# Kernel tuning notes

Measured on AMD Instinct MI355X. Metric: run time of the kernel, lower is better.

## Reference

```python
import jax, jax.numpy as jnp
import numpy as np

SIMS = 16
AMP = 1.0  # cfg['attention_amplifier']


def setup_inputs() -> dict:
    key = jax.random.key(0)
    k1, k2, k3 = jax.random.split(key, 3)
    B, F = 32, 2048
    data = jax.random.normal(k1, (B * SIMS, F), dtype=jnp.float32)
    attention = jax.random.normal(k2, (B * SIMS, F), dtype=jnp.float32)
    W = jax.random.normal(k3, (SIMS, 2 * SIMS), dtype=jnp.float32) * (1.0 / np.sqrt(2 * SIMS))
    b = jnp.zeros((SIMS,), dtype=jnp.float32)
    return {"data": data, "attention": attention, "W": W, "b": b}


def reference(data, attention, W, b):
    s = SIMS
    B = data.shape[0] // s
    inputs = data.reshape(B, s, -1)            # [B, s, F]
    attn_in = attention.reshape(B, s, -1)      # [B, s, G]
    # bmm(inputs^T, attention) -> [B, F, G]
    a = jnp.einsum('bsf,bsg->bfg', inputs, attn_in)
    a = jax.nn.log_softmax(a, axis=1)          # log_softmax over F dim (dim=1)
    # bmm(a, attention^T) -> [B, F, s]
    a = jnp.einsum('bfg,bsg->bfs', a, attn_in)
    concat = jnp.concatenate([jnp.swapaxes(a, 1, 2), inputs], axis=1)  # [B, 2s, F]
    concat = jnp.swapaxes(concat, 1, 2).reshape(-1, 2 * s)             # [B*F, 2s]
    gate = jax.nn.sigmoid(concat @ W.T + b)    # [B*F, s]
    # output.t().contiguous().view(data.shape): [s, B*F] row-major -> [B*s, F]
    gate = gate.T.reshape(data.shape)
    return gate * data * AMP
```

## Files before the change

kernel.cpp:

```cpp
#include <hip/hip_runtime.h>
#include <math.h>

#define LOG2E 1.44269504088896340736f
#define LN2   0.69314718055994530942f

typedef _Float16 half8 __attribute__((ext_vector_type(8)));
typedef float f32x4v __attribute__((ext_vector_type(4)));

#define AROW 24

template <bool ATOMIC>
__global__ __launch_bounds__(256, 4) void kA(const float* __restrict__ data,
                                             const float* __restrict__ attn,
                                             float* __restrict__ Lout) {
    __shared__ _Float16 AhB[128 * AROW];
    __shared__ _Float16 AlB[128 * AROW];
    const int tid = threadIdx.x;
    const int lin = blockIdx.x;
    const int b = lin & 31, fb = (lin >> 5) & 3, gb = lin >> 7;
    const int wave = tid >> 6, lane = tid & 63;
    const int n = lane & 15, q = lane >> 4;
    const int s0 = (q & 1) * 8;

    const float* Tb = attn + (size_t)b * 16 * 2048;
    half8 B1[2], B2[2];
#pragma unroll
    for (int ct = 0; ct < 2; ++ct) {
        const int g = gb * 128 + wave * 32 + ct * 16 + n;
        half8 bh, bl;
#pragma unroll
        for (int j = 0; j < 8; ++j) {
            float x = Tb[(size_t)(s0 + j) * 2048 + g] * LOG2E;
            _Float16 h = (_Float16)x;
            _Float16 l = (_Float16)(x - (float)h);
            bh[j] = h;
            bl[j] = (q < 2) ? l : (_Float16)0.0f;
        }
        B1[ct] = bh;
        B2[ct] = bl;
    }

    f32x4v cs0 = {0.f, 0.f, 0.f, 0.f}, cs1 = {0.f, 0.f, 0.f, 0.f};

    const float* Ab = data + (size_t)b * 16 * 2048 + fb * 512;
    const int fst = tid & 127;
    const int sh  = (tid >> 7) * 8;
    const _Float16* aptr = ((q < 2) ? AhB : AlB) + n * AROW + s0;

    float x[8];
#pragma unroll
    for (int j = 0; j < 8; ++j) x[j] = Ab[(size_t)(sh + j) * 2048 + fst];

    for (int chunk = 0; chunk < 4; ++chunk) {
        half8 hv, lv;
#pragma unroll
        for (int j = 0; j < 8; ++j) {
            float v = x[j];
            _Float16 h = (_Float16)v;
            hv[j] = h;
            lv[j] = (_Float16)(v - (float)h);
        }
        __syncthreads();
        *(half8*)(AhB + fst * AROW + sh) = hv;
        *(half8*)(AlB + fst * AROW + sh) = lv;
        __syncthreads();

        if (chunk < 3) {
            const float* Ac = Ab + (chunk + 1) * 128;
#pragma unroll
            for (int j = 0; j < 8; ++j) x[j] = Ac[(size_t)(sh + j) * 2048 + fst];
        }

#pragma unroll
        for (int rt = 0; rt < 8; ++rt) {
            half8 af = *(const half8*)(aptr + rt * 16 * AROW);
            f32x4v C = {0.f, 0.f, 0.f, 0.f};
            C = __builtin_amdgcn_mfma_f32_16x16x32_f16(af, B1[0], C, 0, 0, 0);
            C = __builtin_amdgcn_mfma_f32_16x16x32_f16(af, B2[0], C, 0, 0, 0);
            cs0[0] += __builtin_amdgcn_exp2f(C[0]);
            cs0[1] += __builtin_amdgcn_exp2f(C[1]);
            cs0[2] += __builtin_amdgcn_exp2f(C[2]);
            cs0[3] += __builtin_amdgcn_exp2f(C[3]);
            f32x4v D = {0.f, 0.f, 0.f, 0.f};
            D = __builtin_amdgcn_mfma_f32_16x16x32_f16(af, B1[1], D, 0, 0, 0);
            D = __builtin_amdgcn_mfma_f32_16x16x32_f16(af, B2[1], D, 0, 0, 0);
            cs1[0] += __builtin_amdgcn_exp2f(D[0]);
            cs1[1] += __builtin_amdgcn_exp2f(D[1]);
            cs1[2] += __builtin_amdgcn_exp2f(D[2]);
            cs1[3] += __builtin_amdgcn_exp2f(D[3]);
        }
    }

    float v0 = cs0[0] + cs0[1] + cs0[2] + cs0[3];
    float v1 = cs1[0] + cs1[1] + cs1[2] + cs1[3];
    v0 += __shfl_xor(v0, 16);
    v0 += __shfl_xor(v0, 32);
    v1 += __shfl_xor(v1, 16);
    v1 += __shfl_xor(v1, 32);
    if (q == 0) {
        const int g = gb * 128 + wave * 32 + n;
        if (ATOMIC) {
            atomicAdd(&Lout[(size_t)b * 2048 + g], v0);
            atomicAdd(&Lout[(size_t)b * 2048 + g + 16], v1);
        } else {
            Lout[((size_t)fb * 32 + b) * 2048 + g] = v0;
            Lout[((size_t)fb * 32 + b) * 2048 + g + 16] = v1;
        }
    }
}

#define TP2 132
__global__ __launch_bounds__(256) void kTail(const float* __restrict__ attn,
                                             const float* __restrict__ Lpart, int nparts,
                                             float* __restrict__ Mpart,
                                             float* __restrict__ cpart) {
    __shared__ float Tsh[16 * TP2];
    __shared__ float Lsh[128];
    __shared__ float red[16][17];
    const int tid = threadIdx.x;
    const int seg = blockIdx.x, b = blockIdx.y;
    const int g0 = seg * 128;

    {
        const int gcol = tid & 127, sh = (tid >> 7) * 8;
#pragma unroll
        for (int j = 0; j < 8; ++j) {
            const int s = sh + j;
            Tsh[s * TP2 + gcol] = attn[(size_t)(b * 16 + s) * 2048 + g0 + gcol];
        }
    }
    if (tid < 128) {
        float sum = 0.f;
        for (int p = 0; p < nparts; ++p)
            sum += Lpart[((size_t)p * 32 + b) * 2048 + g0 + tid];
        Lsh[tid] = LN2 * __builtin_amdgcn_logf(sum);
    }
    __syncthreads();

    {
        const int t = tid & 15, i = tid >> 4;
        float acc = 0.f;
#pragma unroll
        for (int k = 0; k < 2; ++k) {
            float4 l  = *(const float4*)(Lsh + i * 8 + k * 4);
            float4 tv = *(const float4*)(Tsh + t * TP2 + i * 8 + k * 4);
            acc += l.x * tv.x + l.y * tv.y + l.z * tv.z + l.w * tv.w;
        }
        red[t][i] = acc;
    }
    __syncthreads();
    if (tid < 16) {
        float s = 0.f;
#pragma unroll
        for (int k = 0; k < 16; ++k) s += red[tid][k];
        cpart[((size_t)seg * 32 + b) * 16 + tid] = s;
    }

    {
        const int s = tid >> 4, t = tid & 15;
        float a0 = 0.f, a1 = 0.f;
#pragma unroll 4
        for (int qk = 0; qk < 16; ++qk) {
            float4 x = *(const float4*)(Tsh + s * TP2 + qk * 8);
            float4 y = *(const float4*)(Tsh + t * TP2 + qk * 8);
            a0 += x.x * y.x + x.y * y.y + x.z * y.z + x.w * y.w;
            float4 x2 = *(const float4*)(Tsh + s * TP2 + qk * 8 + 4);
            float4 y2 = *(const float4*)(Tsh + t * TP2 + qk * 8 + 4);
            a1 += x2.x * y2.x + x2.y * y2.y + x2.z * y2.z + x2.w * y2.w;
        }
        Mpart[((size_t)seg * 32 + b) * 256 + tid] = a0 + a1;
    }
}

#define NSEG 16
__global__ __launch_bounds__(256) void kC2(const float* __restrict__ data,
                                           const float* __restrict__ Mpart,
                                           const float* __restrict__ cpart,
                                           const float* __restrict__ W,
                                           const float* __restrict__ bias,
                                           float* __restrict__ out) {
    __shared__ float Msh[256];
    __shared__ float csh[16];
    __shared__ float Vsh[256];
    __shared__ float w0sh[16];
    const int tid = threadIdx.x;
    const int b = blockIdx.y;
    const int f = blockIdx.x * 128 + (tid & 127);
    const int jh = tid >> 7;

    {
        float m = 0.f;
#pragma unroll
        for (int p = 0; p < NSEG; ++p) m += Mpart[((size_t)p * 32 + b) * 256 + tid];
        Msh[tid] = m;
        if (tid < 16) {
            float c = 0.f;
#pragma unroll
            for (int p = 0; p < NSEG; ++p) c += cpart[((size_t)p * 32 + b) * 16 + tid];
            csh[tid] = c;
        }
    }
    __syncthreads();
    {
        const int s = tid >> 4, j = tid & 15;
        float acc = 0.f;
#pragma unroll
        for (int t = 0; t < 16; ++t) acc += Msh[s * 16 + t] * W[j * 32 + t];
        Vsh[s * 16 + j] = acc + W[j * 32 + 16 + s];
        if (s == 0) {
            float w0 = 0.f;
#pragma unroll
            for (int t = 0; t < 16; ++t) w0 += csh[t] * W[j * 32 + t];
            w0sh[j] = bias[j] - w0;
        }
    }
    __syncthreads();

    float As[16];
#pragma unroll
    for (int s = 0; s < 16; ++s)
        As[s] = data[(size_t)(b * 16 + s) * 2048 + f];
#pragma unroll
    for (int jj = 0; jj < 8; ++jj) {
        const int j = jh * 8 + jj;
        float p = w0sh[j];
#pragma unroll
        for (int s = 0; s < 16; ++s) p += As[s] * Vsh[s * 16 + j];
        float e = __builtin_amdgcn_exp2f(-LOG2E * p);
        float gate = __builtin_amdgcn_rcpf(1.0f + e);
        size_t r = (size_t)(j * 32 + b) * 2048 + f;
        out[r] = gate * data[r];
    }
}

extern "C" void kernel_launch(void* const* d_in, const int* in_sizes, int n_in,
                              void* d_out, int out_size, void* d_ws, size_t ws_size,
                              hipStream_t stream) {
    const float* data = (const float*)d_in[0];
    const float* attn = (const float*)d_in[1];
    const float* W    = (const float*)d_in[2];
    const float* bias = (const float*)d_in[3];
    float* out = (float*)d_out;
    float* ws  = (float*)d_ws;

    const size_t LP = 4 * 32 * 2048;
    const size_t MP = NSEG * 32 * 256;
    const size_t CP = NSEG * 32 * 16;
    const size_t need_big = LP + MP + CP;

    if (ws_size >= need_big * sizeof(float)) {
        float* Lpart = ws;
        float* Mpart = ws + LP;
        float* cpart = Mpart + MP;
        kA<false><<<dim3(2048, 1, 1), 256, 0, stream>>>(data, attn, Lpart);
        kTail<<<dim3(16, 32), 256, 0, stream>>>(attn, Lpart, 4, Mpart, cpart);
        kC2<<<dim3(16, 32), 256, 0, stream>>>(data, Mpart, cpart, W, bias, out);
    } else {
        float* Lsum  = ws;
        float* Mpart = ws + 65536;
        float* cpart = Mpart + MP;
        hipMemsetAsync(Lsum, 0, 65536 * sizeof(float), stream);
        kA<true><<<dim3(2048, 1, 1), 256, 0, stream>>>(data, attn, Lsum);
        kTail<<<dim3(16, 32), 256, 0, stream>>>(attn, Lsum, 1, Mpart, cpart);
        kC2<<<dim3(16, 32), 256, 0, stream>>>(data, Mpart, cpart, W, bias, out);
    }
}
```

Before: 94.09 us.

## Precompute fp16 hi/lo MFMA fragments in a prep kernel, drop LDS staging in kA

Adds a prep kernel that splits data and attention into fp16 hi/lo parts once and writes them to workspace, already laid out as MFMA fragments. The main kA kernel then loads fragments straight from global memory, with no LDS staging, no barriers and no per-block conversion. Before, each block redid the split for the data and attention tiles it read, so the same conversions ran many times across blocks. The cost is an extra launch and extra global traffic for the fragment buffers, plus a larger workspace requirement. The old LDS kernel is kept as the fallback when workspace is small.

```diff
diff --git a/kernel.cpp b/kernel.cpp
--- a/kernel.cpp
+++ b/kernel.cpp
@@ -7,12 +7,119 @@
 typedef _Float16 half8 __attribute__((ext_vector_type(8)));
 typedef float f32x4v __attribute__((ext_vector_type(4)));
 
+__global__ __launch_bounds__(256) void kPrep(const float* __restrict__ data,
+                                             const float* __restrict__ attn,
+                                             _Float16* __restrict__ Afrag,
+                                             _Float16* __restrict__ Tfrag) {
+    const int tid = threadIdx.x;
+    const int b = blockIdx.y;
+    const int f = blockIdx.x * 256 + tid;
+
+    _Float16 h16[16], l16[16];
+#pragma unroll
+    for (int s = 0; s < 16; ++s) {
+        float v = data[(size_t)(b * 16 + s) * 2048 + f];
+        _Float16 h = (_Float16)v;
+        h16[s] = h;
+        l16[s] = (_Float16)(v - (float)h);
+    }
+    {
+        const int fb = f >> 9, c = (f >> 7) & 3, rt = (f >> 4) & 7, n = f & 15;
+        _Float16* dst = Afrag + ((size_t)((b * 4 + fb) * 32 + c * 8 + rt)) * 512 + n * 8;
+#pragma unroll
+        for (int qq = 0; qq < 4; ++qq) {
+            const _Float16* src = (qq < 2) ? h16 : l16;
+            const int s0 = (qq & 1) * 8;
+            half8 v;
+#pragma unroll
+            for (int j = 0; j < 8; ++j) v[j] = src[s0 + j];
+            *(half8*)(dst + qq * 128) = v;
+        }
+    }
+
+    _Float16 th[16], tl[16];
+#pragma unroll
+    for (int s = 0; s < 16; ++s) {
+        float v = attn[(size_t)(b * 16 + s) * 2048 + f] * LOG2E;
+        _Float16 h = (_Float16)v;
+        th[s] = h;
+        tl[s] = (_Float16)(v - (float)h);
+    }
+#pragma unroll
+    for (int p = 0; p < 4; ++p) {
+        const _Float16* src = (p < 2) ? th : tl;
+        const int s0 = (p & 1) * 8;
+        half8 v;
+#pragma unroll
+        for (int j = 0; j < 8; ++j) v[j] = src[s0 + j];
+        *(half8*)(Tfrag + ((size_t)(b * 4 + p) * 2048 + f) * 8) = v;
+    }
+}
+
+template <bool ATOMIC>
+__global__ __launch_bounds__(256, 4) void kA(const _Float16* __restrict__ Afrag,
+                                             const _Float16* __restrict__ Tfrag,
+                                             float* __restrict__ Lout) {
+    const int tid = threadIdx.x;
+    const int lin = blockIdx.x;
+    const int gb = lin & 15, b = (lin >> 4) & 31, fb = lin >> 9;
+    const int wave = tid >> 6, lane = tid & 63;
+    const int n = lane & 15, q = lane >> 4;
+
+    half8 B1[2], B2[2];
+    const half8 zero = {};
+#pragma unroll
+    for (int ct = 0; ct < 2; ++ct) {
+        const int g = gb * 128 + wave * 32 + ct * 16 + n;
+        B1[ct] = *(const half8*)(Tfrag + ((size_t)(b * 4 + (q & 1)) * 2048 + g) * 8);
+        half8 b2 = *(const half8*)(Tfrag + ((size_t)(b * 4 + 2 + (q & 1)) * 2048 + g) * 8);
+        B2[ct] = (q < 2) ? b2 : zero;
+    }
+
+    f32x4v cs0 = {0.f, 0.f, 0.f, 0.f}, cs1 = {0.f, 0.f, 0.f, 0.f};
+    const _Float16* Ab = Afrag + ((size_t)((b * 4 + fb) * 32)) * 512 + lane * 8;
+
+#pragma unroll 4
+    for (int rr = 0; rr < 32; ++rr) {
+        half8 af = *(const half8*)(Ab + (size_t)rr * 512);
+        f32x4v C = {0.f, 0.f, 0.f, 0.f};
+        C = __builtin_amdgcn_mfma_f32_16x16x32_f16(af, B1[0], C, 0, 0, 0);
+        C = __builtin_amdgcn_mfma_f32_16x16x32_f16(af, B2[0], C, 0, 0, 0);
+        cs0[0] += __builtin_amdgcn_exp2f(C[0]);
+        cs0[1] += __builtin_amdgcn_exp2f(C[1]);
+        cs0[2] += __builtin_amdgcn_exp2f(C[2]);
+        cs0[3] += __builtin_amdgcn_exp2f(C[3]);
+        f32x4v D = {0.f, 0.f, 0.f, 0.f};
+        D = __builtin_amdgcn_mfma_f32_16x16x32_f16(af, B1[1], D, 0, 0, 0);
+        D = __builtin_amdgcn_mfma_f32_16x16x32_f16(af, B2[1], D, 0, 0, 0);
+        cs1[0] += __builtin_amdgcn_exp2f(D[0]);
+        cs1[1] += __builtin_amdgcn_exp2f(D[1]);
+        cs1[2] += __builtin_amdgcn_exp2f(D[2]);
+        cs1[3] += __builtin_amdgcn_exp2f(D[3]);
+    }
+
+    float v0 = cs0[0] + cs0[1] + cs0[2] + cs0[3];
+    float v1 = cs1[0] + cs1[1] + cs1[2] + cs1[3];
+    v0 += __shfl_xor(v0, 16);
+    v0 += __shfl_xor(v0, 32);
+    v1 += __shfl_xor(v1, 16);
+    v1 += __shfl_xor(v1, 32);
+    if (q == 0) {
+        const int g = gb * 128 + wave * 32 + n;
+        if (ATOMIC) {
+            atomicAdd(&Lout[(size_t)b * 2048 + g], v0);
+            atomicAdd(&Lout[(size_t)b * 2048 + g + 16], v1);
+        } else {
+            Lout[((size_t)fb * 32 + b) * 2048 + g] = v0;
+            Lout[((size_t)fb * 32 + b) * 2048 + g + 16] = v1;
+        }
+    }
+}
+
 #define AROW 24
-
-template <bool ATOMIC>
-__global__ __launch_bounds__(256, 4) void kA(const float* __restrict__ data,
-                                             const float* __restrict__ attn,
-                                             float* __restrict__ Lout) {
+__global__ __launch_bounds__(256, 4) void kA_lds(const float* __restrict__ data,
+                                                 const float* __restrict__ attn,
+                                                 float* __restrict__ Lout) {
     __shared__ _Float16 AhB[128 * AROW];
     __shared__ _Float16 AlB[128 * AROW];
     const int tid = threadIdx.x;
@@ -41,10 +148,9 @@
     }
 
     f32x4v cs0 = {0.f, 0.f, 0.f, 0.f}, cs1 = {0.f, 0.f, 0.f, 0.f};
-
     const float* Ab = data + (size_t)b * 16 * 2048 + fb * 512;
     const int fst = tid & 127;
-    const int sh  = (tid >> 7) * 8;
+    const int sh = (tid >> 7) * 8;
     const _Float16* aptr = ((q < 2) ? AhB : AlB) + n * AROW + s0;
 
     float x[8];
@@ -64,13 +170,11 @@
         *(half8*)(AhB + fst * AROW + sh) = hv;
         *(half8*)(AlB + fst * AROW + sh) = lv;
         __syncthreads();
-
         if (chunk < 3) {
             const float* Ac = Ab + (chunk + 1) * 128;
 #pragma unroll
             for (int j = 0; j < 8; ++j) x[j] = Ac[(size_t)(sh + j) * 2048 + fst];
         }
-
 #pragma unroll
         for (int rt = 0; rt < 8; ++rt) {
             half8 af = *(const half8*)(aptr + rt * 16 * AROW);
@@ -99,13 +203,8 @@
     v1 += __shfl_xor(v1, 32);
     if (q == 0) {
         const int g = gb * 128 + wave * 32 + n;
-        if (ATOMIC) {
-            atomicAdd(&Lout[(size_t)b * 2048 + g], v0);
-            atomicAdd(&Lout[(size_t)b * 2048 + g + 16], v1);
-        } else {
-            Lout[((size_t)fb * 32 + b) * 2048 + g] = v0;
-            Lout[((size_t)fb * 32 + b) * 2048 + g + 16] = v1;
-        }
+        atomicAdd(&Lout[(size_t)b * 2048 + g], v0);
+        atomicAdd(&Lout[(size_t)b * 2048 + g + 16], v1);
     }
 }
 
@@ -161,9 +260,9 @@
         float a0 = 0.f, a1 = 0.f;
 #pragma unroll 4
         for (int qk = 0; qk < 16; ++qk) {
-            float4 x = *(const float4*)(Tsh + s * TP2 + qk * 8);
-            float4 y = *(const float4*)(Tsh + t * TP2 + qk * 8);
-            a0 += x.x * y.x + x.y * y.y + x.z * y.z + x.w * y.w;
+            float4 xv = *(const float4*)(Tsh + s * TP2 + qk * 8);
+            float4 yv = *(const float4*)(Tsh + t * TP2 + qk * 8);
+            a0 += xv.x * yv.x + xv.y * yv.y + xv.z * yv.z + xv.w * yv.w;
             float4 x2 = *(const float4*)(Tsh + s * TP2 + qk * 8 + 4);
             float4 y2 = *(const float4*)(Tsh + t * TP2 + qk * 8 + 4);
             a1 += x2.x * y2.x + x2.y * y2.y + x2.z * y2.z + x2.w * y2.w;
@@ -246,13 +345,18 @@
     const size_t LP = 4 * 32 * 2048;
     const size_t MP = NSEG * 32 * 256;
     const size_t CP = NSEG * 32 * 16;
-    const size_t need_big = LP + MP + CP;
+    const size_t AF = 1048576;
+    const size_t TF = 1048576;
+    const size_t need_big = LP + MP + CP + AF + TF;
 
     if (ws_size >= need_big * sizeof(float)) {
         float* Lpart = ws;
         float* Mpart = ws + LP;
         float* cpart = Mpart + MP;
-        kA<false><<<dim3(2048, 1, 1), 256, 0, stream>>>(data, attn, Lpart);
+        _Float16* Afrag = (_Float16*)(cpart + CP);
+        _Float16* Tfrag = (_Float16*)(cpart + CP + AF);
+        kPrep<<<dim3(8, 32), 256, 0, stream>>>(data, attn, Afrag, Tfrag);
+        kA<false><<<dim3(2048, 1, 1), 256, 0, stream>>>(Afrag, Tfrag, Lpart);
         kTail<<<dim3(16, 32), 256, 0, stream>>>(attn, Lpart, 4, Mpart, cpart);
         kC2<<<dim3(16, 32), 256, 0, stream>>>(data, Mpart, cpart, W, bias, out);
     } else {
@@ -260,7 +364,7 @@
         float* Mpart = ws + 65536;
         float* cpart = Mpart + MP;
         hipMemsetAsync(Lsum, 0, 65536 * sizeof(float), stream);
-        kA<true><<<dim3(2048, 1, 1), 256, 0, stream>>>(data, attn, Lsum);
+        kA_lds<<<dim3(2048, 1, 1), 256, 0, stream>>>(data, attn, Lsum);
         kTail<<<dim3(16, 32), 256, 0, stream>>>(attn, Lsum, 1, Mpart, cpart);
         kC2<<<dim3(16, 32), 256, 0, stream>>>(data, Mpart, cpart, W, bias, out);
     }
```

After: 96.38 us. +2.4%, slower.
